# Optimization experiments

Hardware: AMD Instinct MI355X
Metric: run time of the kernel (lower is better)

The kernel has to match this reference:

```python
import jax, jax.numpy as jnp
import numpy as np

B, S, D, H, HD = 2, 2048, 1024, 16, 64
SCALE = HD ** (-0.5)

def setup_inputs() -> dict:
    key = jax.random.key(0)
    ks = jax.random.split(key, 11)
    f = jax.random.normal
    return {
        "K_in": f(ks[0], (B, S, D), jnp.float32),
        "V_in": f(ks[1], (B, S, D), jnp.float32),
        "Q_in": f(ks[2], (B, S, D), jnp.float32),
        "Wk": f(ks[3], (H, D, HD), jnp.float32) * 0.02,
        "bk": f(ks[4], (H, HD), jnp.float32) * 0.02,
        "Wq": f(ks[5], (H, D, HD), jnp.float32) * 0.02,
        "bq": f(ks[6], (H, HD), jnp.float32) * 0.02,
        "Wv": f(ks[7], (H, D, HD), jnp.float32) * 0.02,
        "bv": f(ks[8], (H, HD), jnp.float32) * 0.02,
        "Wp": f(ks[9], (D, D), jnp.float32) * 0.02,
        "bp": f(ks[10], (D,), jnp.float32) * 0.02,
    }

def reference(K_in, V_in, Q_in, Wk, bk, Wq, bq, Wv, bv, Wp, bp):
    # Per-head linear projections (batched over heads): [B,H,S,HD]
    K = jnp.einsum('bsd,hde->bhse', K_in, Wk) + bk[None, :, None, :]
    Q = jnp.einsum('bsd,hde->bhse', Q_in, Wq) + bq[None, :, None, :]
    V = jnp.einsum('bsd,hde->bhse', V_in, Wv) + bv[None, :, None, :]
    # Attention scores [B,H,S,S], softmax over keys
    W = jax.nn.softmax(jnp.einsum('bhqe,bhke->bhqk', Q, K) * SCALE, axis=-1)
    val = jnp.einsum('bhqk,bhke->bhqe', W, V)            # [B,H,S,HD]
    # Concatenate heads along feature dim -> [B,S,H*HD] = [B,S,D]
    concat = jnp.transpose(val, (0, 2, 1, 3)).reshape(K_in.shape[0], K_in.shape[1], -1)
    return concat @ Wp.T + bp
```

## Files before the change

kernel.cpp:

```cpp
#include <hip/hip_runtime.h>
#include <hip/hip_bf16.h>
#include <math.h>

typedef float f32x4 __attribute__((ext_vector_type(4)));
typedef short s16x8 __attribute__((ext_vector_type(8)));
typedef unsigned short us16x4 __attribute__((ext_vector_type(4)));
typedef unsigned short us16x8 __attribute__((ext_vector_type(8)));
typedef unsigned int u32x2 __attribute__((ext_vector_type(2)));

#define MFMA16(a, b, c) __builtin_amdgcn_mfma_f32_16x16x32_bf16(a, b, c, 0, 0, 0)

static constexpr int B_ = 2, S_ = 2048, D_ = 1024, H_ = 16, HD_ = 64;
static constexpr float QSCALE = 0.125f * 1.44269504088896340736f;

__device__ __forceinline__ unsigned short f2bf(float f) {
    unsigned int u = __builtin_bit_cast(unsigned int, f);
    u += 0x7fffu + ((u >> 16) & 1);
    return (unsigned short)(u >> 16);
}

#if defined(__has_builtin) && __has_builtin(__builtin_amdgcn_cvt_pk_bf16_f32)
typedef __bf16 bf16x2v __attribute__((ext_vector_type(2)));
__device__ __forceinline__ unsigned int pk_bf16(float a, float b) {
    return __builtin_bit_cast(unsigned int, __builtin_amdgcn_cvt_pk_bf16_f32(a, b));
}
#else
__device__ __forceinline__ unsigned int pk_bf16(float a, float b) {
    return ((unsigned int)f2bf(a)) | (((unsigned int)f2bf(b)) << 16);
}
#endif

__device__ __forceinline__ void glds16(const unsigned short* g, unsigned short* l) {
    __builtin_amdgcn_global_load_lds(
        (const __attribute__((address_space(1))) void*)g,
        (__attribute__((address_space(3))) void*)l, 16, 0, 0);
}

__global__ __launch_bounds__(256) void conv3(const float* __restrict__ s0,
                                             const float* __restrict__ s1,
                                             const float* __restrict__ s2,
                                             unsigned short* __restrict__ d0,
                                             unsigned short* __restrict__ d1,
                                             unsigned short* __restrict__ d2) {
    const int z = blockIdx.z;
    const float* src = (z == 0) ? s0 : (z == 1) ? s1 : s2;
    unsigned short* dst = (z == 0) ? d0 : (z == 1) ? d1 : d2;
    int i = (blockIdx.x * 256 + threadIdx.x) * 8;
    f32x4 a = *(const f32x4*)&src[i];
    f32x4 b = *(const f32x4*)&src[i + 4];
    s16x8 o;
#pragma unroll
    for (int j = 0; j < 4; j++) { o[j] = (short)f2bf(a[j]); o[4 + j] = (short)f2bf(b[j]); }
    *(s16x8*)&dst[i] = o;
}

__global__ __launch_bounds__(256) void conv_bf16(const float* __restrict__ src,
                                                 unsigned short* __restrict__ dst) {
    int i = (blockIdx.x * 256 + threadIdx.x) * 8;
    f32x4 a = *(const f32x4*)&src[i];
    f32x4 b = *(const f32x4*)&src[i + 4];
    s16x8 o;
#pragma unroll
    for (int j = 0; j < 4; j++) { o[j] = (short)f2bf(a[j]); o[4 + j] = (short)f2bf(b[j]); }
    *(s16x8*)&dst[i] = o;
}

__global__ __launch_bounds__(256) void transpose_w3(const float* __restrict__ W0,
                                                    const float* __restrict__ W1,
                                                    const float* __restrict__ W2,
                                                    unsigned short* __restrict__ Wt3) {
    const int z = blockIdx.z;
    const float* W = (z == 0) ? W0 : (z == 1) ? W1 : W2;
    unsigned short* dst = Wt3 + ((size_t)z << 20);
    const int h = blockIdx.x >> 2, dg = blockIdx.x & 3;
    const int lane = threadIdx.x & 63, w = threadIdx.x >> 6;
    const float* Wh = W + ((size_t)h << 16);
#pragma unroll
    for (int it = 0; it < 8; it++) {
        int d0 = dg * 256 + it * 32 + w * 8;
        us16x8 o;
#pragma unroll
        for (int j = 0; j < 8; j++) o[j] = f2bf(Wh[(d0 + j) * 64 + lane]);
        *(us16x8*)&dst[(size_t)(h * 64 + lane) * 1024 + d0] = o;
    }
}

__device__ __forceinline__ void gemm_core128(const unsigned short* __restrict__ A,
                                             const unsigned short* __restrict__ Bt,
                                             unsigned short* As, unsigned short* Bs,
                                             int m0, int n0, f32x4 acc[4][4]) {
    const int tid = threadIdx.x;
    const int lane = tid & 63;
    const int w = tid >> 6, wm = w & 1, wn = w >> 1;
    const int l16 = lane & 15, quad = lane >> 4;
    const int srow = tid >> 3;
    const int sg = (tid & 7) ^ (srow & 7);
    const unsigned short* Ag = A + (size_t)(m0 + srow) * 1024 + sg * 8;
    const unsigned short* Bg = Bt + (size_t)(n0 + srow) * 1024 + sg * 8;
    unsigned short* Al = As + tid * 8;
    unsigned short* Bl = Bs + tid * 8;
    const int xo = (l16 & 7);

    for (int k0 = 0; k0 < 1024; k0 += 64) {
        __syncthreads();
#pragma unroll
        for (int c = 0; c < 4; c++) {
            glds16(Ag + (size_t)c * 32 * 1024 + k0, Al + c * 2048);
            glds16(Bg + (size_t)c * 32 * 1024 + k0, Bl + c * 2048);
        }
        __syncthreads();
#pragma unroll
        for (int kc = 0; kc < 2; kc++) {
            s16x8 bf[4];
#pragma unroll
            for (int nt = 0; nt < 4; nt++)
                bf[nt] = *(const s16x8*)&Bs[(wn * 64 + nt * 16 + l16) * 64 +
                                            (((kc * 4 + quad) ^ xo) * 8)];
#pragma unroll
            for (int mt = 0; mt < 4; mt++) {
                s16x8 af = *(const s16x8*)&As[(wm * 64 + mt * 16 + l16) * 64 +
                                              (((kc * 4 + quad) ^ xo) * 8)];
#pragma unroll
                for (int nt = 0; nt < 4; nt++)
                    acc[mt][nt] = MFMA16(af, bf[nt], acc[mt][nt]);
            }
        }
    }
}

__global__ __launch_bounds__(256) void gemm_qkv(const unsigned short* __restrict__ Qc,
                                                const unsigned short* __restrict__ Kc,
                                                const unsigned short* __restrict__ Vc,
                                                const unsigned short* __restrict__ Wt3,
                                                const float* __restrict__ bq,
                                                const float* __restrict__ bk,
                                                const float* __restrict__ bv,
                                                unsigned short* __restrict__ Qr,
                                                unsigned short* __restrict__ Kr,
                                                unsigned short* __restrict__ Vt) {
    __shared__ unsigned short As[128 * 64];
    __shared__ unsigned short Bs[128 * 64];
    const int z = blockIdx.z;
    const unsigned short* A = (z == 0) ? Qc : (z == 1) ? Kc : Vc;
    const unsigned short* Bt = Wt3 + ((size_t)z << 20);
    const float* bias = (z == 0) ? bq : (z == 1) ? bk : bv;
    const int m0 = blockIdx.y * 128, n0 = blockIdx.x * 128;

    f32x4 acc[4][4] = {};
    gemm_core128(A, Bt, As, Bs, m0, n0, acc);

    const int tid = threadIdx.x;
    const int lane = tid & 63, w = tid >> 6;
    const int wm = w & 1, wn = w >> 1;
    const int l16 = lane & 15, quad = lane >> 4;
    const float scl = (z == 0) ? QSCALE : 1.0f;

    __syncthreads();
    unsigned short* T = ((w < 2) ? As : Bs) + (w & 1) * 4096;
#pragma unroll
    for (int mt = 0; mt < 4; mt++)
#pragma unroll
        for (int nt = 0; nt < 4; nt++) {
            int nl = nt * 16 + l16;
            float bsv = bias[n0 + wn * 64 + nl];
#pragma unroll
            for (int r = 0; r < 4; r++) {
                int ml = mt * 16 + quad * 4 + r;
                unsigned short val = f2bf((acc[mt][nt][r] + bsv) * scl);
                int row = (z == 2) ? nl : ml;
                int col = (z == 2) ? ml : nl;
                T[row * 64 + (((col >> 3) ^ (row & 7)) * 8) + (col & 7)] = val;
            }
        }
#pragma unroll
    for (int it = 0; it < 8; it++) {
        int rr = it * 8 + (lane >> 3);
        int g = lane & 7;
        us16x8 vv = *(const us16x8*)&T[rr * 64 + ((g ^ (rr & 7)) * 8)];
        if (z == 2) {
            int n = n0 + wn * 64 + rr;
            int mb = m0 + wm * 64 + g * 8;
            int b = mb >> 11, s = mb & 2047;
            *(us16x8*)&Vt[(((size_t)(b * H_ + (n >> 6))) * HD_ + (n & 63)) * S_ + s] = vv;
        } else {
            unsigned short* dst = z ? Kr : Qr;
            *(us16x8*)&dst[(size_t)(m0 + wm * 64 + rr) * 1024 + n0 + wn * 64 + g * 8] = vv;
        }
    }
}

__global__ __launch_bounds__(256) void gemm_out(const unsigned short* __restrict__ A,
                                                const unsigned short* __restrict__ Bt,
                                                const float* __restrict__ bias,
                                                float* __restrict__ C) {
    __shared__ unsigned short As[128 * 64];
    __shared__ unsigned short Bs[64 * 64];
    const int tid = threadIdx.x;
    const int lane = tid & 63;
    const int w = tid >> 6, wm = w & 1, wn = w >> 1;
    const int l16 = lane & 15, quad = lane >> 4;
    const int m0 = blockIdx.y * 128, n0 = blockIdx.x * 64;
    const int srow = tid >> 3;
    const int sg = (tid & 7) ^ (srow & 7);
    const unsigned short* Ag = A + (size_t)(m0 + srow) * 1024 + sg * 8;
    const unsigned short* Bg = Bt + (size_t)(n0 + srow) * 1024 + sg * 8;
    unsigned short* Al = As + tid * 8;
    unsigned short* Bl = Bs + tid * 8;
    const int xo = l16 & 7;

    f32x4 acc[4][2] = {};
    for (int k0 = 0; k0 < 1024; k0 += 64) {
        __syncthreads();
#pragma unroll
        for (int c = 0; c < 4; c++)
            glds16(Ag + (size_t)c * 32 * 1024 + k0, Al + c * 2048);
#pragma unroll
        for (int c = 0; c < 2; c++)
            glds16(Bg + (size_t)c * 32 * 1024 + k0, Bl + c * 2048);
        __syncthreads();
#pragma unroll
        for (int kc = 0; kc < 2; kc++) {
            s16x8 bf[2];
#pragma unroll
            for (int nt = 0; nt < 2; nt++)
                bf[nt] = *(const s16x8*)&Bs[(wn * 32 + nt * 16 + l16) * 64 +
                                            (((kc * 4 + quad) ^ xo) * 8)];
#pragma unroll
            for (int mt = 0; mt < 4; mt++) {
                s16x8 af = *(const s16x8*)&As[(wm * 64 + mt * 16 + l16) * 64 +
                                              (((kc * 4 + quad) ^ xo) * 8)];
#pragma unroll
                for (int nt = 0; nt < 2; nt++)
                    acc[mt][nt] = MFMA16(af, bf[nt], acc[mt][nt]);
            }
        }
    }
    const int lq = quad;
#pragma unroll
    for (int mt = 0; mt < 4; mt++)
#pragma unroll
        for (int nt = 0; nt < 2; nt++)
#pragma unroll
            for (int r = 0; r < 4; r++) {
                int mg = m0 + wm * 64 + mt * 16 + lq * 4 + r;
                int ng = n0 + wn * 32 + nt * 16 + l16;
                C[(size_t)mg * 1024 + ng] = acc[mt][nt][r] + bias[ng];
            }
}

__global__ __launch_bounds__(256) void flash_attn(const unsigned short* __restrict__ Qr,
                                                  const unsigned short* __restrict__ Kr,
                                                  const unsigned short* __restrict__ Vt,
                                                  unsigned short* __restrict__ Cc) {
    __shared__ unsigned short Ks[64 * 64];
    __shared__ unsigned short Vs[64 * 64];
    constexpr int LDT = 72;
    __shared__ unsigned short P4[4][16 * LDT];

    const int tid = threadIdx.x;
    const int lane = tid & 63, w = tid >> 6;
    const int l16 = lane & 15, quad = lane >> 4;
    const int bh = blockIdx.x, q0 = blockIdx.y * 64;
    const int b = bh >> 4, h = bh & 15;
    const int s_q = q0 + w * 16 + l16;

    const unsigned short* Qp = Qr + ((size_t)(b * S_ + s_q)) * D_ + h * HD_;
    s16x8 aq0 = *(const s16x8*)&Qp[quad * 8];
    s16x8 aq1 = *(const s16x8*)&Qp[32 + quad * 8];

    const int srow = tid >> 3;
    const int sg = (tid & 7) ^ (srow & 7);
    const unsigned short* kg = Kr + ((size_t)(b * S_ + srow)) * D_ + h * HD_ + sg * 8;
    const unsigned short* vg = Vt + (((size_t)(b * H_ + h)) * HD_ + srow) * S_ + sg * 8;
    unsigned short* Kl = Ks + tid * 8;
    unsigned short* Vl = Vs + tid * 8;
    unsigned short* Pw = P4[w];
    const int pbase = l16 * LDT + quad * 4;
    const int xo = l16 & 7;

    float l_part = 0.f;
    f32x4 o[4] = {};
    const f32x4 z4 = {0.f, 0.f, 0.f, 0.f};

    for (int k0 = 0; k0 < S_; k0 += 64) {
        __syncthreads();
        glds16(kg, Kl);
        glds16(kg + (size_t)32 * D_, Kl + 2048);
        glds16(vg, Vl);
        glds16(vg + (size_t)32 * S_, Vl + 2048);
        kg += (size_t)64 * D_;
        vg += 64;
        __syncthreads();

#pragma unroll
        for (int g = 0; g < 4; g++) {
            int row = g * 16 + l16;
            s16x8 kb0 = *(const s16x8*)&Ks[row * 64 + ((quad ^ xo) * 8)];
            s16x8 kb1 = *(const s16x8*)&Ks[row * 64 + (((4 + quad) ^ xo) * 8)];
            f32x4 sc = MFMA16(kb0, aq0, z4);
            sc = MFMA16(kb1, aq1, sc);
            float e0 = exp2f(sc[0]), e1 = exp2f(sc[1]);
            float e2 = exp2f(sc[2]), e3 = exp2f(sc[3]);
            l_part += (e0 + e1) + (e2 + e3);
            u32x2 pv;
            pv[0] = pk_bf16(e0, e1);
            pv[1] = pk_bf16(e2, e3);
            *(u32x2*)&Pw[pbase + g * 16] = pv;
        }
        s16x8 pB0 = *(const s16x8*)&Pw[l16 * LDT + quad * 8];
        s16x8 pB1 = *(const s16x8*)&Pw[l16 * LDT + 32 + quad * 8];
#pragma unroll
        for (int t = 0; t < 4; t++) {
            int row = t * 16 + l16;
            s16x8 v0 = *(const s16x8*)&Vs[row * 64 + ((quad ^ xo) * 8)];
            s16x8 v1 = *(const s16x8*)&Vs[row * 64 + (((4 + quad) ^ xo) * 8)];
            o[t] = MFMA16(v0, pB0, o[t]);
            o[t] = MFMA16(v1, pB1, o[t]);
        }
    }
    float l = l_part;
    l += __shfl_xor(l, 16);
    l += __shfl_xor(l, 32);
    float rinv = 1.0f / l;
    unsigned short* Cp = Cc + ((size_t)(b * S_ + s_q)) * D_ + h * HD_;
#pragma unroll
    for (int t = 0; t < 4; t++) {
        u32x2 ov;
        ov[0] = pk_bf16(o[t][0] * rinv, o[t][1] * rinv);
        ov[1] = pk_bf16(o[t][2] * rinv, o[t][3] * rinv);
        *(u32x2*)&Cp[t * 16 + quad * 4] = ov;
    }
}

extern "C" void kernel_launch(void* const* d_in, const int* in_sizes, int n_in,
                              void* d_out, int out_size, void* d_ws, size_t ws_size,
                              hipStream_t stream) {
    const float* K_in = (const float*)d_in[0];
    const float* V_in = (const float*)d_in[1];
    const float* Q_in = (const float*)d_in[2];
    const float* Wk   = (const float*)d_in[3];
    const float* bk   = (const float*)d_in[4];
    const float* Wq   = (const float*)d_in[5];
    const float* bq   = (const float*)d_in[6];
    const float* Wv   = (const float*)d_in[7];
    const float* bv   = (const float*)d_in[8];
    const float* Wp   = (const float*)d_in[9];
    const float* bp   = (const float*)d_in[10];

    unsigned short* ws16 = (unsigned short*)d_ws;
    const size_t MC = 1u << 20;
    unsigned short* Qc  = ws16;
    unsigned short* Kc  = Qc + 4 * MC;
    unsigned short* Vc  = Kc + 4 * MC;
    unsigned short* Wt3 = Vc + 4 * MC;
    unsigned short* Qr  = Wt3 + 3 * MC;
    unsigned short* Kr  = Qr + 4 * MC;
    unsigned short* Vt  = Kr + 4 * MC;
    unsigned short* Cc  = Qc;
    unsigned short* Wpb = Wt3;

    conv3<<<dim3(2048, 1, 3), 256, 0, stream>>>(Q_in, K_in, V_in, Qc, Kc, Vc);
    transpose_w3<<<dim3(64, 1, 3), 256, 0, stream>>>(Wq, Wk, Wv, Wt3);

    gemm_qkv<<<dim3(8, 32, 3), 256, 0, stream>>>(Qc, Kc, Vc, Wt3, bq, bk, bv, Qr, Kr, Vt);

    conv_bf16<<<512, 256, 0, stream>>>(Wp, Wpb);

    flash_attn<<<dim3(32, 32), 256, 0, stream>>>(Qr, Kr, Vt, Cc);

    gemm_out<<<dim3(16, 32), 256, 0, stream>>>(Cc, Wpb, bp, (float*)d_out);
}
```

Before: 260.2 us.

## Double-buffer K tiles and overlap V load with QK compute in flash attention

The flash attention loop now double-buffers K in shared memory, prefetching the next K tile while the current one is used. The V tile load is issued at the start of each iteration and only awaited, via explicit s_waitcnt and barrier, just before the PV MFMAs, so it overlaps the QK and exp work. Wave priority hints (s_setprio) are added around the MFMA sections. The extra K buffer raises LDS use, and the hand-written waitcnt counts depend on the order in which loads are issued.

New measurement: 260.0 us. No clear change (-0.1%).

```diff
diff --git a/kernel.cpp b/kernel.cpp
--- a/kernel.cpp
+++ b/kernel.cpp
@@ -252,7 +252,7 @@
                                                   const unsigned short* __restrict__ Kr,
                                                   const unsigned short* __restrict__ Vt,
                                                   unsigned short* __restrict__ Cc) {
-    __shared__ unsigned short Ks[64 * 64];
+    __shared__ unsigned short Ks[2][64 * 64];
     __shared__ unsigned short Vs[64 * 64];
     constexpr int LDT = 72;
     __shared__ unsigned short P4[4][16 * LDT];
@@ -265,38 +265,49 @@
     const int s_q = q0 + w * 16 + l16;
 
     const unsigned short* Qp = Qr + ((size_t)(b * S_ + s_q)) * D_ + h * HD_;
-    s16x8 aq0 = *(const s16x8*)&Qp[quad * 8];
-    s16x8 aq1 = *(const s16x8*)&Qp[32 + quad * 8];
 
     const int srow = tid >> 3;
     const int sg = (tid & 7) ^ (srow & 7);
     const unsigned short* kg = Kr + ((size_t)(b * S_ + srow)) * D_ + h * HD_ + sg * 8;
     const unsigned short* vg = Vt + (((size_t)(b * H_ + h)) * HD_ + srow) * S_ + sg * 8;
-    unsigned short* Kl = Ks + tid * 8;
     unsigned short* Vl = Vs + tid * 8;
     unsigned short* Pw = P4[w];
     const int pbase = l16 * LDT + quad * 4;
     const int xo = l16 & 7;
 
+    glds16(kg, &Ks[0][tid * 8]);
+    glds16(kg + (size_t)32 * D_, &Ks[0][tid * 8 + 2048]);
+    kg += (size_t)64 * D_;
+
+    s16x8 aq0 = *(const s16x8*)&Qp[quad * 8];
+    s16x8 aq1 = *(const s16x8*)&Qp[32 + quad * 8];
+
     float l_part = 0.f;
     f32x4 o[4] = {};
     const f32x4 z4 = {0.f, 0.f, 0.f, 0.f};
 
-    for (int k0 = 0; k0 < S_; k0 += 64) {
-        __syncthreads();
-        glds16(kg, Kl);
-        glds16(kg + (size_t)32 * D_, Kl + 2048);
+    asm volatile("s_waitcnt vmcnt(0) lgkmcnt(0)\n\ts_barrier" ::: "memory");
+
+    int cur = 0;
+    for (int t = 0; t < 32; ++t) {
+        const int last = (t == 31);
         glds16(vg, Vl);
         glds16(vg + (size_t)32 * S_, Vl + 2048);
-        kg += (size_t)64 * D_;
         vg += 64;
-        __syncthreads();
-
+        if (!last) {
+            unsigned short* Kn = &Ks[cur ^ 1][tid * 8];
+            glds16(kg, Kn);
+            glds16(kg + (size_t)32 * D_, Kn + 2048);
+            kg += (size_t)64 * D_;
+        }
+
+        const unsigned short* Kc_ = &Ks[cur][0];
+        __builtin_amdgcn_s_setprio(1);
 #pragma unroll
         for (int g = 0; g < 4; g++) {
             int row = g * 16 + l16;
-            s16x8 kb0 = *(const s16x8*)&Ks[row * 64 + ((quad ^ xo) * 8)];
-            s16x8 kb1 = *(const s16x8*)&Ks[row * 64 + (((4 + quad) ^ xo) * 8)];
+            s16x8 kb0 = *(const s16x8*)&Kc_[row * 64 + ((quad ^ xo) * 8)];
+            s16x8 kb1 = *(const s16x8*)&Kc_[row * 64 + (((4 + quad) ^ xo) * 8)];
             f32x4 sc = MFMA16(kb0, aq0, z4);
             sc = MFMA16(kb1, aq1, sc);
             float e0 = exp2f(sc[0]), e1 = exp2f(sc[1]);
@@ -307,17 +318,29 @@
             pv[1] = pk_bf16(e2, e3);
             *(u32x2*)&Pw[pbase + g * 16] = pv;
         }
+        __builtin_amdgcn_s_setprio(0);
         s16x8 pB0 = *(const s16x8*)&Pw[l16 * LDT + quad * 8];
         s16x8 pB1 = *(const s16x8*)&Pw[l16 * LDT + 32 + quad * 8];
-#pragma unroll
-        for (int t = 0; t < 4; t++) {
-            int row = t * 16 + l16;
+
+        if (!last)
+            asm volatile("s_waitcnt vmcnt(2)\n\ts_barrier" ::: "memory");
+        else
+            asm volatile("s_waitcnt vmcnt(0)\n\ts_barrier" ::: "memory");
+
+        __builtin_amdgcn_s_setprio(1);
+#pragma unroll
+        for (int tt = 0; tt < 4; tt++) {
+            int row = tt * 16 + l16;
             s16x8 v0 = *(const s16x8*)&Vs[row * 64 + ((quad ^ xo) * 8)];
             s16x8 v1 = *(const s16x8*)&Vs[row * 64 + (((4 + quad) ^ xo) * 8)];
-            o[t] = MFMA16(v0, pB0, o[t]);
-            o[t] = MFMA16(v1, pB1, o[t]);
-        }
-    }
+            o[tt] = MFMA16(v0, pB0, o[tt]);
+            o[tt] = MFMA16(v1, pB1, o[tt]);
+        }
+        __builtin_amdgcn_s_setprio(0);
+        asm volatile("s_waitcnt vmcnt(0) lgkmcnt(0)\n\ts_barrier" ::: "memory");
+        cur ^= 1;
+    }
+
     float l = l_part;
     l += __shfl_xor(l, 16);
     l += __shfl_xor(l, 32);
```
